# Kernel optimization log

Hardware: AMD Instinct MI355X
Metric: run time of the kernel (lower is better)

## Reference

```python
import jax, jax.numpy as jnp
import numpy as np

T, B, D, W = 1024, 8, 512, 32

def setup_inputs() -> dict:
    key = jax.random.key(0)
    k1, k2, k3 = jax.random.split(key, 3)
    inputs = jax.random.normal(k1, (T, B, D), dtype=jnp.float32)
    weight_W = jax.random.uniform(k2, (D, D), dtype=jnp.float32, minval=-0.1, maxval=0.1)
    weight_proj = jax.random.uniform(k3, (D, 1), dtype=jnp.float32, minval=-0.1, maxval=0.1)
    return {"inputs": inputs, "weight_W": weight_W, "weight_proj": weight_proj,
            "attention_width": W}

def reference(inputs, weight_W, weight_proj, attention_width):
    # inputs: [T, B, D]. For step i < w: passthrough. For i >= w: attend over
    # window inputs[i-w : i] (current step EXCLUDED, matching the original).
    Tn, Bn, Dn = inputs.shape
    w = attention_width
    # window gather indices: row t corresponds to output step i = t + w,
    # covering timesteps [i-w, i) == [t, t+w)
    idx = jnp.arange(Tn - w)[:, None] + jnp.arange(w)          # [T-w, w]
    windows = inputs[idx]                                       # [T-w, w, B, D]
    u = jnp.tanh(jnp.einsum('twbd,de->twbe', windows, weight_W))  # [T-w, w, B, D]
    scores = jnp.einsum('twbd,d->twb', u, weight_proj[:, 0])      # [T-w, w, B]
    # NOTE: original uses legacy nn.Softmax() on a [w, B] tensor, whose implicit
    # dim is 1 (the batch dim). We reproduce that math faithfully: softmax over B.
    a = jax.nn.softmax(scores, axis=-1)                           # [T-w, w, B]
    attended = jnp.einsum('twb,twbd->tbd', a, windows)            # [T-w, B, D]
    return jnp.concatenate([inputs[:w], attended], axis=0)       # [T, B, D]
```

## Files before the change

### kernel.cpp

```cpp
#include <hip/hip_runtime.h>
#include <cstdint>

namespace {
constexpr int T = 1024;
constexpr int B = 8;
constexpr int D = 512;
constexpr int W = 32;
constexpr int M = T * B;
}

using half8  = __attribute__((ext_vector_type(8))) _Float16;
using f32x16 = __attribute__((ext_vector_type(16))) float;

__device__ __forceinline__ void gload16(const void* g, void* l) {
    __builtin_amdgcn_global_load_lds(
        (const __attribute__((address_space(1))) void*)g,
        (__attribute__((address_space(3))) void*)l, 16, 0, 0);
}

__device__ __forceinline__ float fast_tanh(float x) {
    float e = __expf(2.f * x);
    return 1.f - 2.f / (e + 1.f);
}

__global__ __launch_bounds__(256) void prep_merged(
    const float* __restrict__ X, const float* __restrict__ Wm,
    _Float16* __restrict__ Ah, _Float16* __restrict__ Bt)
{
    __shared__ float tile[64][65];
    const int tid = threadIdx.x;
    const int bid = blockIdx.x;

    {
        const int c = bid * 256 + tid;
        const float4* X4 = reinterpret_cast<const float4*>(X);
        const float4 v0 = X4[(size_t)c * 2];
        const float4 v1 = X4[(size_t)c * 2 + 1];
        half8 h;
        h[0] = (_Float16)v0.x; h[1] = (_Float16)v0.y; h[2] = (_Float16)v0.z; h[3] = (_Float16)v0.w;
        h[4] = (_Float16)v1.x; h[5] = (_Float16)v1.y; h[6] = (_Float16)v1.z; h[7] = (_Float16)v1.w;
        *reinterpret_cast<half8*>(Ah + (size_t)c * 8) = h;
    }

    if (bid < 64) {
        const int bd = bid & 7;
        const int be = bid >> 3;
        const int r  = tid >> 2;
        const int c0 = (tid & 3) * 16;
        const float* src = Wm + (size_t)(be * 64 + r) * 512 + bd * 64 + c0;
#pragma unroll
        for (int j = 0; j < 16; j += 4) {
            const float4 v = *reinterpret_cast<const float4*>(src + j);
            tile[r][c0 + j]     = v.x;
            tile[r][c0 + j + 1] = v.y;
            tile[r][c0 + j + 2] = v.z;
            tile[r][c0 + j + 3] = v.w;
        }
        __syncthreads();
        const int dd = tid >> 2;
        const int e0 = (tid & 3) * 16;
        half8 h0, h1;
#pragma unroll
        for (int j = 0; j < 8; ++j)  h0[j] = (_Float16)tile[e0 + j][dd];
#pragma unroll
        for (int j = 0; j < 8; ++j)  h1[j] = (_Float16)tile[e0 + 8 + j][dd];
        _Float16* dst = Bt + (size_t)(bd * 64 + dd) * 512 + be * 64 + e0;
        *reinterpret_cast<half8*>(dst)     = h0;
        *reinterpret_cast<half8*>(dst + 8) = h1;
    }
}

__global__ __launch_bounds__(256) void gemm_scores(
    const _Float16* __restrict__ Ah, const _Float16* __restrict__ Bt,
    const float* __restrict__ proj, float* __restrict__ spart)
{
    __shared__ char lds_buf[49152];

    const int tid  = threadIdx.x;
    const int lane = tid & 63;
    const int wv   = tid >> 6;
    const int wm   = wv >> 1;
    const int wn   = wv & 1;
    const int hi   = lane >> 5;
    const int l31  = lane & 31;
    const int l7   = lane & 7;

    const int bid  = blockIdx.x;
    const int wgid = (bid & 7) * 64 + (bid >> 3);
    const int mb   = wgid >> 2;
    const int nb   = wgid & 3;
    const int m0   = mb * 64;
    const int n0   = nb * 128;

    const int wbase = __builtin_amdgcn_readfirstlane(tid & ~63);

    f32x16 acc0 = {}, acc1 = {};

    auto stage = [&](int bufi, int kt) {
        char* abase = lds_buf + bufi * 24576;
        char* bbase = abase + 8192;
        const int kbase = kt * 64;
#pragma unroll
        for (int i = 0; i < 2; ++i) {
            const int c   = i * 256 + tid;
            const int row = c >> 3;
            const int ch  = c & 7;
            const int koff = kbase + ((ch ^ (row & 7)) << 3);
            gload16(Ah + (size_t)(m0 + row) * 512 + koff,
                    abase + (size_t)(i * 256 + wbase) * 16);
        }
#pragma unroll
        for (int i = 0; i < 4; ++i) {
            const int c   = i * 256 + tid;
            const int row = c >> 3;
            const int ch  = c & 7;
            const int koff = kbase + ((ch ^ (row & 7)) << 3);
            gload16(Bt + (size_t)(n0 + row) * 512 + koff,
                    bbase + (size_t)(i * 256 + wbase) * 16);
        }
    };

    stage(0, 0);

    int cur = 0;
    const int rowA  = wm * 32 + l31;
    const int colB0 = wn * 64 + l31;
    const int colB1 = colB0 + 32;

    for (int kt = 0; kt < 8; ++kt) {
        if (kt < 7) {
            stage(cur ^ 1, kt + 1);
            asm volatile("s_waitcnt vmcnt(6)" ::: "memory");
        } else {
            asm volatile("s_waitcnt vmcnt(0)" ::: "memory");
        }
        __syncthreads();

        const char* Ab = lds_buf + cur * 24576;
        const char* Bb = Ab + 8192;

        half8 af[4], bf0[4], bf1[4];
#pragma unroll
        for (int s = 0; s < 4; ++s) {
            const int ch = ((2 * s + hi) ^ l7) << 4;
            af[s]  = *reinterpret_cast<const half8*>(Ab + rowA  * 128 + ch);
            bf0[s] = *reinterpret_cast<const half8*>(Bb + colB0 * 128 + ch);
            bf1[s] = *reinterpret_cast<const half8*>(Bb + colB1 * 128 + ch);
        }
        __builtin_amdgcn_s_setprio(1);
#pragma unroll
        for (int s = 0; s < 4; ++s) {
            acc0 = __builtin_amdgcn_mfma_f32_32x32x16_f16(af[s], bf0[s], acc0, 0, 0, 0);
            acc1 = __builtin_amdgcn_mfma_f32_32x32x16_f16(af[s], bf1[s], acc1, 0, 0, 0);
        }
        __builtin_amdgcn_s_setprio(0);

        __syncthreads();
        cur ^= 1;
    }

    const float pj0 = proj[n0 + wn * 64 + l31];
    const float pj1 = proj[n0 + wn * 64 + 32 + l31];
    float* sp = spart + (size_t)(nb * 2 + wn) * M;

#pragma unroll
    for (int reg = 0; reg < 16; ++reg) {
        float v0 = fast_tanh(acc0[reg]) * pj0 + fast_tanh(acc1[reg]) * pj1;
#pragma unroll
        for (int msk = 1; msk < 32; msk <<= 1)
            v0 += __shfl_xor(v0, msk, 64);
        if (l31 == 0) {
            const int rl = (reg & 3) + 8 * (reg >> 2) + 4 * hi;
            sp[m0 + wm * 32 + rl] = v0;
        }
    }
}

__global__ __launch_bounds__(256) void attend_kernel(
    const float* __restrict__ X, const _Float16* __restrict__ Ah,
    const float* __restrict__ spart, float* __restrict__ out)
{
    __shared__ char lds[49152];
    _Float16* W_lds = reinterpret_cast<_Float16*>(lds);
    float*    p_lds = reinterpret_cast<float*>(lds + 48128);

    const int vb  = blockIdx.x;
    const int tid = threadIdx.x;
    const int ih  = vb & 1;
    const int b   = (vb >> 1) & 7;
    const int ig  = vb >> 4;
    const int i0  = ig * 32 + ih * 16;

    if (ig == 0) {
        const float4* X4 = reinterpret_cast<const float4*>(X);
        float4* O4 = reinterpret_cast<float4*>(out);
        for (int idx = tid; idx < 16 * 128; idx += 256) {
            const int r = idx >> 7;
            const int c = idx & 127;
            const size_t off = (size_t)((i0 + r) * 8 + b) * 128 + c;
            O4[off] = X4[off];
        }
        return;
    }

    const int tau0 = i0 - 32;
    const int lane = tid & 63;
    const int wbase = __builtin_amdgcn_readfirstlane(tid & ~63);

    {
        const _Float16* src = Ah + (size_t)(tau0 * 8 + b) * 512;
#pragma unroll
        for (int it = 0; it < 12; ++it) {
            const int cbase = it * 256 + wbase;
            if (cbase < 3008) {
                const int c  = cbase + lane;
                const int r  = c >> 6;
                const int ch = c & 63;
                gload16(src + (size_t)r * 4096 + ch * 8,
                        (char*)W_lds + (size_t)cbase * 16);
            }
        }
    }

    const int bj = tid & 7;
#pragma unroll
    for (int half = 0; half < 2; ++half) {
        const int lt = (tid >> 3) + half * 32;
        if (lt < 47) {
            float s = 0.f;
#pragma unroll
            for (int g = 0; g < 8; ++g)
                s += spart[(size_t)g * M + (size_t)(tau0 + lt) * 8 + bj];
            float mx = s;
#pragma unroll
            for (int msk = 1; msk < 8; msk <<= 1)
                mx = fmaxf(mx, __shfl_xor(mx, msk, 64));
            const float e = __expf(s - mx);
            float sum = e;
#pragma unroll
            for (int msk = 1; msk < 8; msk <<= 1)
                sum += __shfl_xor(sum, msk, 64);
            if (bj == b) p_lds[lt] = e / sum;
        }
    }

    asm volatile("s_waitcnt vmcnt(0)" ::: "memory");
    __syncthreads();

    const int rg = tid >> 6;
    const int u0 = rg * 4;
    float acc[4][8];
#pragma unroll
    for (int q = 0; q < 4; ++q)
#pragma unroll
        for (int j = 0; j < 8; ++j) acc[q][j] = 0.f;

    auto apply = [&](int u, int qlo, int qhi) {
        const int lt = u0 + u;
        const float pw = p_lds[lt];
        const half8 h = *reinterpret_cast<const half8*>(
            W_lds + (size_t)lt * 512 + lane * 8);
        float hf[8];
#pragma unroll
        for (int j = 0; j < 8; ++j) hf[j] = (float)h[j];
        for (int q = qlo; q <= qhi; ++q)
#pragma unroll
            for (int j = 0; j < 8; ++j)
                acc[q][j] = fmaf(pw, hf[j], acc[q][j]);
    };

#pragma unroll
    for (int u = 0; u < 3; ++u)  apply(u, 0, u);
    for (int u = 3; u < 32; ++u) apply(u, 0, 3);
#pragma unroll
    for (int u = 32; u < 35; ++u) apply(u, u - 31, 3);

#pragma unroll
    for (int q = 0; q < 4; ++q) {
        float4* O4 = reinterpret_cast<float4*>(
            out + (size_t)((i0 + u0 + q) * 8 + b) * 512 + lane * 8);
        O4[0] = float4{acc[q][0], acc[q][1], acc[q][2], acc[q][3]};
        O4[1] = float4{acc[q][4], acc[q][5], acc[q][6], acc[q][7]};
    }
}

extern "C" void kernel_launch(void* const* d_in, const int* in_sizes, int n_in,
                              void* d_out, int out_size, void* d_ws, size_t ws_size,
                              hipStream_t stream)
{
    const float* X    = (const float*)d_in[0];
    const float* Wm   = (const float*)d_in[1];
    const float* proj = (const float*)d_in[2];
    float* out = (float*)d_out;

    _Float16* Ah   = (_Float16*)d_ws;
    _Float16* Bt   = Ah + (size_t)M * D;
    float*    sprt = (float*)(Bt + (size_t)D * D);

    prep_merged<<<2048, 256, 0, stream>>>(X, Wm, Ah, Bt);
    gemm_scores<<<512, 256, 0, stream>>>(Ah, Bt, proj, sprt);
    attend_kernel<<<(T / W) * B * 2, 256, 0, stream>>>(X, Ah, sprt, out);
}
```

Before: 36.79 us.

## Fuse fp32-to-fp16 conversion of inputs into GEMM A-tile staging

```diff
diff --git a/kernel.cpp b/kernel.cpp
--- a/kernel.cpp
+++ b/kernel.cpp
@@ -23,56 +23,42 @@
     return 1.f - 2.f / (e + 1.f);
 }
 
-__global__ __launch_bounds__(256) void prep_merged(
-    const float* __restrict__ X, const float* __restrict__ Wm,
-    _Float16* __restrict__ Ah, _Float16* __restrict__ Bt)
+__global__ __launch_bounds__(256) void prep_slim(
+    const float* __restrict__ Wm, _Float16* __restrict__ Bt)
 {
     __shared__ float tile[64][65];
     const int tid = threadIdx.x;
     const int bid = blockIdx.x;
-
-    {
-        const int c = bid * 256 + tid;
-        const float4* X4 = reinterpret_cast<const float4*>(X);
-        const float4 v0 = X4[(size_t)c * 2];
-        const float4 v1 = X4[(size_t)c * 2 + 1];
-        half8 h;
-        h[0] = (_Float16)v0.x; h[1] = (_Float16)v0.y; h[2] = (_Float16)v0.z; h[3] = (_Float16)v0.w;
-        h[4] = (_Float16)v1.x; h[5] = (_Float16)v1.y; h[6] = (_Float16)v1.z; h[7] = (_Float16)v1.w;
-        *reinterpret_cast<half8*>(Ah + (size_t)c * 8) = h;
-    }
-
-    if (bid < 64) {
-        const int bd = bid & 7;
-        const int be = bid >> 3;
-        const int r  = tid >> 2;
-        const int c0 = (tid & 3) * 16;
-        const float* src = Wm + (size_t)(be * 64 + r) * 512 + bd * 64 + c0;
-#pragma unroll
-        for (int j = 0; j < 16; j += 4) {
-            const float4 v = *reinterpret_cast<const float4*>(src + j);
-            tile[r][c0 + j]     = v.x;
-            tile[r][c0 + j + 1] = v.y;
-            tile[r][c0 + j + 2] = v.z;
-            tile[r][c0 + j + 3] = v.w;
-        }
-        __syncthreads();
-        const int dd = tid >> 2;
-        const int e0 = (tid & 3) * 16;
-        half8 h0, h1;
-#pragma unroll
-        for (int j = 0; j < 8; ++j)  h0[j] = (_Float16)tile[e0 + j][dd];
-#pragma unroll
-        for (int j = 0; j < 8; ++j)  h1[j] = (_Float16)tile[e0 + 8 + j][dd];
-        _Float16* dst = Bt + (size_t)(bd * 64 + dd) * 512 + be * 64 + e0;
-        *reinterpret_cast<half8*>(dst)     = h0;
-        *reinterpret_cast<half8*>(dst + 8) = h1;
-    }
+    const int bd = bid & 7;
+    const int be = bid >> 3;
+    const int r  = tid >> 2;
+    const int c0 = (tid & 3) * 16;
+    const float* src = Wm + (size_t)(be * 64 + r) * 512 + bd * 64 + c0;
+#pragma unroll
+    for (int j = 0; j < 16; j += 4) {
+        const float4 v = *reinterpret_cast<const float4*>(src + j);
+        tile[r][c0 + j]     = v.x;
+        tile[r][c0 + j + 1] = v.y;
+        tile[r][c0 + j + 2] = v.z;
+        tile[r][c0 + j + 3] = v.w;
+    }
+    __syncthreads();
+    const int dd = tid >> 2;
+    const int e0 = (tid & 3) * 16;
+    half8 h0, h1;
+#pragma unroll
+    for (int j = 0; j < 8; ++j)  h0[j] = (_Float16)tile[e0 + j][dd];
+#pragma unroll
+    for (int j = 0; j < 8; ++j)  h1[j] = (_Float16)tile[e0 + 8 + j][dd];
+    _Float16* dst = Bt + (size_t)(bd * 64 + dd) * 512 + be * 64 + e0;
+    *reinterpret_cast<half8*>(dst)     = h0;
+    *reinterpret_cast<half8*>(dst + 8) = h1;
 }
 
 __global__ __launch_bounds__(256) void gemm_scores(
-    const _Float16* __restrict__ Ah, const _Float16* __restrict__ Bt,
-    const float* __restrict__ proj, float* __restrict__ spart)
+    const float* __restrict__ X, const _Float16* __restrict__ Bt,
+    const float* __restrict__ proj, float* __restrict__ spart,
+    _Float16* __restrict__ Ah)
 {
     __shared__ char lds_buf[49152];
 
@@ -91,24 +77,30 @@
     const int nb   = wgid & 3;
     const int m0   = mb * 64;
     const int n0   = nb * 128;
+    const bool storeAh = (nb == 0);
 
     const int wbase = __builtin_amdgcn_readfirstlane(tid & ~63);
 
+    const int rowA0c = (tid) >> 3,        chA0 = tid & 7;
+    const int rowA1c = (256 + tid) >> 3,  chA1 = (256 + tid) & 7;
+    const int swzA0  = (chA0 ^ (rowA0c & 7)) << 3;
+    const int swzA1  = (chA1 ^ (rowA1c & 7)) << 3;
+
     f32x16 acc0 = {}, acc1 = {};
-
-    auto stage = [&](int bufi, int kt) {
-        char* abase = lds_buf + bufi * 24576;
-        char* bbase = abase + 8192;
+    float4 areg[4];
+
+    auto issueA = [&](int kt) {
         const int kbase = kt * 64;
-#pragma unroll
-        for (int i = 0; i < 2; ++i) {
-            const int c   = i * 256 + tid;
-            const int row = c >> 3;
-            const int ch  = c & 7;
-            const int koff = kbase + ((ch ^ (row & 7)) << 3);
-            gload16(Ah + (size_t)(m0 + row) * 512 + koff,
-                    abase + (size_t)(i * 256 + wbase) * 16);
-        }
+        const float* s0 = X + (size_t)(m0 + rowA0c) * 512 + kbase + swzA0;
+        const float* s1 = X + (size_t)(m0 + rowA1c) * 512 + kbase + swzA1;
+        areg[0] = *reinterpret_cast<const float4*>(s0);
+        areg[1] = *reinterpret_cast<const float4*>(s0 + 4);
+        areg[2] = *reinterpret_cast<const float4*>(s1);
+        areg[3] = *reinterpret_cast<const float4*>(s1 + 4);
+    };
+    auto issueB = [&](int bufi, int kt) {
+        char* bbase = lds_buf + bufi * 24576 + 8192;
+        const int kbase = kt * 64;
 #pragma unroll
         for (int i = 0; i < 4; ++i) {
             const int c   = i * 256 + tid;
@@ -119,8 +111,28 @@
                     bbase + (size_t)(i * 256 + wbase) * 16);
         }
     };
-
-    stage(0, 0);
+    auto writeA = [&](int bufi, int kt) {
+        char* abase = lds_buf + bufi * 24576;
+        half8 h0, h1;
+#pragma unroll
+        for (int j = 0; j < 4; ++j) {
+            h0[j]     = (_Float16)areg[0][j];
+            h0[4 + j] = (_Float16)areg[1][j];
+            h1[j]     = (_Float16)areg[2][j];
+            h1[4 + j] = (_Float16)areg[3][j];
+        }
+        *reinterpret_cast<half8*>(abase + (size_t)tid * 16)         = h0;
+        *reinterpret_cast<half8*>(abase + (size_t)(256 + tid) * 16) = h1;
+        if (storeAh) {
+            const int kbase = kt * 64;
+            *reinterpret_cast<half8*>(Ah + (size_t)(m0 + rowA0c) * 512 + kbase + swzA0) = h0;
+            *reinterpret_cast<half8*>(Ah + (size_t)(m0 + rowA1c) * 512 + kbase + swzA1) = h1;
+        }
+    };
+
+    issueA(0);
+    issueB(0, 0);
+    writeA(0, 0);
 
     int cur = 0;
     const int rowA  = wm * 32 + l31;
@@ -129,8 +141,9 @@
 
     for (int kt = 0; kt < 8; ++kt) {
         if (kt < 7) {
-            stage(cur ^ 1, kt + 1);
-            asm volatile("s_waitcnt vmcnt(6)" ::: "memory");
+            issueA(kt + 1);
+            issueB(cur ^ 1, kt + 1);
+            asm volatile("s_waitcnt vmcnt(8)" ::: "memory");
         } else {
             asm volatile("s_waitcnt vmcnt(0)" ::: "memory");
         }
@@ -155,6 +168,10 @@
         }
         __builtin_amdgcn_s_setprio(0);
 
+        if (kt < 7) {
+            asm volatile("s_waitcnt vmcnt(4)" ::: "memory");
+            writeA(cur ^ 1, kt + 1);
+        }
         __syncthreads();
         cur ^= 1;
     }
@@ -297,7 +314,7 @@
     _Float16* Bt   = Ah + (size_t)M * D;
     float*    sprt = (float*)(Bt + (size_t)D * D);
 
-    prep_merged<<<2048, 256, 0, stream>>>(X, Wm, Ah, Bt);
-    gemm_scores<<<512, 256, 0, stream>>>(Ah, Bt, proj, sprt);
+    prep_slim<<<64, 256, 0, stream>>>(Wm, Bt);
+    gemm_scores<<<512, 256, 0, stream>>>(X, Bt, proj, sprt, Ah);
     attend_kernel<<<(T / W) * B * 2, 256, 0, stream>>>(X, Ah, sprt, out);
 }
```

Result: slower. 40.76 us (+10.8%).
